# Optimization experiments

Hardware: AMD Instinct MI355X
Metric: run time of the kernel (lower is better)

Reference implementation:

```python
import jax, jax.numpy as jnp
import numpy as np

NEG = -1e6  # mask fill value used by d2l.sequence_mask


def setup_inputs() -> dict:
    key = jax.random.key(0)
    k1, k2, k3, k4, k5, k6, k7 = jax.random.split(key, 7)
    B, Q, K, DQ, DK, H, DV = 8, 256, 1024, 256, 256, 128, 128
    queries = jax.random.normal(k1, (B, Q, DQ), dtype=jnp.float32)
    keys = jax.random.normal(k2, (B, K, DK), dtype=jnp.float32)
    values = jax.random.normal(k3, (B, K, DV), dtype=jnp.float32)
    valid_lens = jax.random.randint(k4, (B,), 1, K + 1, dtype=jnp.int32)
    # learned params (nn.Linear stores weight as [out, in]; apply as x @ W.T)
    W_q = jax.random.normal(k5, (H, DQ), dtype=jnp.float32) / np.sqrt(DQ)
    W_k = jax.random.normal(k6, (H, DK), dtype=jnp.float32) / np.sqrt(DK)
    w_v = jax.random.normal(k7, (H,), dtype=jnp.float32) / np.sqrt(H)
    return {"queries": queries, "keys": keys, "values": values,
            "valid_lens": valid_lens, "W_q": W_q, "W_k": W_k, "w_v": w_v}


def reference(queries, keys, values, valid_lens, W_q, W_k, w_v):
    # projections
    q = jnp.einsum('bqd,hd->bqh', queries, W_q)   # [B,Q,H]
    k = jnp.einsum('bkd,hd->bkh', keys, W_k)      # [B,K,H]
    # broadcast add + tanh -> [B,Q,K,H] (the fusion-headroom intermediate)
    features = jnp.tanh(q[:, :, None, :] + k[:, None, :, :])
    scores = jnp.einsum('bqkh,h->bqk', features, w_v)  # [B,Q,K]
    # masked softmax: valid_lens is per-batch (dim==1 path)
    klen = scores.shape[-1]
    mask = jnp.arange(klen)[None, None, :] < valid_lens[:, None, None]
    scores = jnp.where(mask, scores, NEG)
    weights = jax.nn.softmax(scores, axis=-1)
    # dropout is identity in eval mode
    return jnp.einsum('bqk,bkv->bqv', weights, values)
```

## Files before the change

### kernel.cpp

```cpp
#include <hip/hip_runtime.h>


#define Bb 8
#define Qn 256
#define Kk 1024
#define Dd 256
#define Hh 128
#define DVv 128

__device__ __forceinline__ float fexp2(float x) { return __builtin_amdgcn_exp2f(x); }
__device__ __forceinline__ float frcp(float x)  { return __builtin_amdgcn_rcpf(x); }

__global__ __launch_bounds__(256)
void repack_w(const float* __restrict__ Wq, const float* __restrict__ Wk,
              float4* __restrict__ Wq4T, float4* __restrict__ Wk4T)
{
    const int blk = blockIdx.x;
    const float* src = (blk < 32) ? Wq : Wk;
    float4*      dst = (blk < 32) ? Wq4T : Wk4T;
    const int idx = (blk & 31) * 256 + threadIdx.x;
    const int g = idx >> 7;
    const int h = idx & 127;
    dst[idx] = *(const float4*)(src + (size_t)h * Dd + g * 4);
}

__global__ __launch_bounds__(512)
void proj_exp_kernel(const float* __restrict__ queries,
                     const float* __restrict__ keys,
                     const float4* __restrict__ Wq4T,
                     const float4* __restrict__ Wk4T,
                     float* __restrict__ EqT,
                     float* __restrict__ EkT)
{
    __shared__ __align__(16) float Xs[16 * 256];
    const int blk = blockIdx.x;
    const float* X; const float4* W4; float* outT; int RB; int i0;
    if (blk < 128) { X = queries; W4 = Wq4T; outT = EqT; RB = Qn; i0 = blk * 16; }
    else           { X = keys;    W4 = Wk4T; outT = EkT; RB = Kk; i0 = (blk - 128) * 16; }
    const int tid = threadIdx.x;
    const int h   = tid & 127;
    const int r4  = __builtin_amdgcn_readfirstlane(tid >> 7);

    {
        const float4* xsrc = (const float4*)(X + (size_t)i0 * Dd);
#pragma unroll
        for (int s = 0; s < 2; ++s) {
            const int idx = tid + 512 * s;
            *(float4*)(Xs + idx * 4) = xsrc[idx];
        }
    }
    __syncthreads();

    float acc[4] = {0.f, 0.f, 0.f, 0.f};
    const float4* wp = W4 + h;
    const float*  xr = Xs + (r4 * 4) * 256;
#pragma unroll 8
    for (int g = 0; g < 64; ++g) {
        const float4 w = wp[(size_t)g * 128];
#pragma unroll
        for (int i = 0; i < 4; ++i) {
            const float4 x = *(const float4*)(xr + i * 256 + g * 4);
            acc[i] = fmaf(x.x, w.x, acc[i]);
            acc[i] = fmaf(x.y, w.y, acc[i]);
            acc[i] = fmaf(x.z, w.z, acc[i]);
            acc[i] = fmaf(x.w, w.w, acc[i]);
        }
    }
    const int b    = i0 / RB;
    const int rloc = (i0 % RB) + r4 * 4;
    float4 o;
    o.x = fexp2(acc[0] * 2.885390082f);
    o.y = fexp2(acc[1] * 2.885390082f);
    o.z = fexp2(acc[2] * 2.885390082f);
    o.w = fexp2(acc[3] * 2.885390082f);
    *(float4*)(outT + (size_t)b * Hh * RB + (size_t)h * RB + rloc) = o;
}

__global__ __launch_bounds__(512, 8)
void score_softmax_pv_kernel(const float* __restrict__ EqT,
                             const float* __restrict__ EkT,
                             const float* __restrict__ wv,
                             const int* __restrict__ valid_lens,
                             const float* __restrict__ values,
                             float* __restrict__ out)
{
    __shared__ __align__(16) float  s_sc[4][Kk];
    __shared__ __align__(16) float  eqsT[4][Hh];
    __shared__ __align__(16) float  w2s[Hh];
    __shared__ __align__(16) float4 s_part[7][4][32];
    __shared__ float s_qmax[4][2];
    __shared__ float s_qsum[4][2];

    const int blk  = blockIdx.x;
    const int b    = blk & 7;
    const int qt   = blk >> 3;
    const int q0   = qt * 4;
    const int len  = valid_lens[b];
    const int tid  = threadIdx.x;
    const int lane = tid & 63;
    const int wave = __builtin_amdgcn_readfirstlane(tid >> 6);

    if (tid < 128) {
        const float4 v = *(const float4*)(EqT + (size_t)b * Hh * Qn + (size_t)tid * Qn + q0);
        eqsT[0][tid] = v.x; eqsT[1][tid] = v.y; eqsT[2][tid] = v.z; eqsT[3][tid] = v.w;
    } else if (tid < 256) {
        w2s[tid - 128] = -2.0f * wv[tid - 128];
    }
    __syncthreads();

    const int kspan = (tid >> 6) << 7;
    if (kspan < len) {
        const float2* ek2 = (const float2*)(EkT + (size_t)b * Hh * Kk) + tid;
        float acc[4][2] = {};
#pragma unroll 2
        for (int hg = 0; hg < 32; ++hg) {
            const int h = hg << 2;
            const float2 e0 = ek2[(size_t)(h + 0) * (Kk / 2)];
            const float2 e1 = ek2[(size_t)(h + 1) * (Kk / 2)];
            const float2 e2 = ek2[(size_t)(h + 2) * (Kk / 2)];
            const float2 e3 = ek2[(size_t)(h + 3) * (Kk / 2)];
            const float4 w4 = *(const float4*)(w2s + h);
#pragma unroll
            for (int q = 0; q < 4; ++q) {
                const float4 q4 = *(const float4*)(&eqsT[q][h]);
                {
                    const float A = fmaf(q4.x, e0.x, 1.f), B = fmaf(q4.y, e1.x, 1.f);
                    const float C = fmaf(q4.z, e2.x, 1.f), E = fmaf(q4.w, e3.x, 1.f);
                    const float AB = A * B, CE = C * E;
                    const float N = fmaf(fmaf(w4.x, B, w4.y * A), CE,
                                         fmaf(w4.z, E, w4.w * C) * AB);
                    acc[q][0] = fmaf(N, frcp(AB * CE), acc[q][0]);
                }
                {
                    const float A = fmaf(q4.x, e0.y, 1.f), B = fmaf(q4.y, e1.y, 1.f);
                    const float C = fmaf(q4.z, e2.y, 1.f), E = fmaf(q4.w, e3.y, 1.f);
                    const float AB = A * B, CE = C * E;
                    const float N = fmaf(fmaf(w4.x, B, w4.y * A), CE,
                                         fmaf(w4.z, E, w4.w * C) * AB);
                    acc[q][1] = fmaf(N, frcp(AB * CE), acc[q][1]);
                }
            }
        }
#pragma unroll
        for (int q = 0; q < 4; ++q)
            *(float2*)(&s_sc[q][tid << 1]) = make_float2(acc[q][0], acc[q][1]);
    }
    __syncthreads();

    {
        const int q    = wave & 3;
        const int half = wave >> 2;
        const int base = half * 512;
        const int hi   = (base + 512 < len) ? base + 512 : len;
        float m = -3.0e38f;
        for (int i = base + lane; i < hi; i += 64) m = fmaxf(m, s_sc[q][i]);
#pragma unroll
        for (int off = 32; off > 0; off >>= 1) m = fmaxf(m, __shfl_xor(m, off));
        if (lane == 0) s_qmax[q][half] = m;
        __syncthreads();
        const float gm = fmaxf(s_qmax[q][0], s_qmax[q][1]);
        float sum = 0.f;
        for (int i = base + lane; i < hi; i += 64) {
            const float p = fexp2((s_sc[q][i] - gm) * 1.44269504f);
            s_sc[q][i] = p;
            sum += p;
        }
#pragma unroll
        for (int off = 32; off > 0; off >>= 1) sum += __shfl_xor(sum, off);
        if (lane == 0) s_qsum[q][half] = sum;
    }
    __syncthreads();

    {
        const int slice = tid >> 5;
        const int l32   = tid & 31;
        const int v4    = l32 << 2;
        const float* vp = values + (size_t)b * Kk * DVv + v4;
        float a[4][4];
#pragma unroll
        for (int q = 0; q < 4; ++q) { a[q][0]=0.f; a[q][1]=0.f; a[q][2]=0.f; a[q][3]=0.f; }
        for (int k = slice; k < len; k += 16) {
            const float4 val = *(const float4*)(vp + (size_t)k * DVv);
            const float w0 = s_sc[0][k], w1 = s_sc[1][k], w2 = s_sc[2][k], w3 = s_sc[3][k];
            a[0][0] = fmaf(w0, val.x, a[0][0]);
            a[0][1] = fmaf(w0, val.y, a[0][1]);
            a[0][2] = fmaf(w0, val.z, a[0][2]);
            a[0][3] = fmaf(w0, val.w, a[0][3]);
            a[1][0] = fmaf(w1, val.x, a[1][0]);
            a[1][1] = fmaf(w1, val.y, a[1][1]);
            a[1][2] = fmaf(w1, val.z, a[1][2]);
            a[1][3] = fmaf(w1, val.w, a[1][3]);
            a[2][0] = fmaf(w2, val.x, a[2][0]);
            a[2][1] = fmaf(w2, val.y, a[2][1]);
            a[2][2] = fmaf(w2, val.z, a[2][2]);
            a[2][3] = fmaf(w2, val.w, a[2][3]);
            a[3][0] = fmaf(w3, val.x, a[3][0]);
            a[3][1] = fmaf(w3, val.y, a[3][1]);
            a[3][2] = fmaf(w3, val.z, a[3][2]);
            a[3][3] = fmaf(w3, val.w, a[3][3]);
        }
#pragma unroll
        for (int q = 0; q < 4; ++q)
#pragma unroll
            for (int x = 0; x < 4; ++x) a[q][x] += __shfl_xor(a[q][x], 32);
        if (wave > 0 && lane < 32) {
#pragma unroll
            for (int q = 0; q < 4; ++q)
                s_part[wave - 1][q][l32] = make_float4(a[q][0], a[q][1], a[q][2], a[q][3]);
        }
        __syncthreads();
        if (wave == 0 && lane < 32) {
#pragma unroll
            for (int q = 0; q < 4; ++q) {
                float r0 = a[q][0], r1 = a[q][1], r2 = a[q][2], r3 = a[q][3];
#pragma unroll
                for (int w = 0; w < 7; ++w) {
                    const float4 p = s_part[w][q][l32];
                    r0 += p.x; r1 += p.y; r2 += p.z; r3 += p.w;
                }
                const float inv = frcp(s_qsum[q][0] + s_qsum[q][1]);
                *(float4*)(out + (size_t)(b * Qn + q0 + q) * DVv + v4) =
                    make_float4(r0 * inv, r1 * inv, r2 * inv, r3 * inv);
            }
        }
    }
}

extern "C" void kernel_launch(void* const* d_in, const int* in_sizes, int n_in,
                              void* d_out, int out_size, void* d_ws, size_t ws_size,
                              hipStream_t stream) {
    (void)in_sizes; (void)n_in; (void)out_size; (void)ws_size;
    const float* queries    = (const float*)d_in[0];
    const float* keys       = (const float*)d_in[1];
    const float* values     = (const float*)d_in[2];
    const int*   valid_lens = (const int*)  d_in[3];
    const float* Wq         = (const float*)d_in[4];
    const float* Wk         = (const float*)d_in[5];
    const float* wvv        = (const float*)d_in[6];
    float* out = (float*)d_out;

    float* Wq4T = (float*)d_ws;
    float* Wk4T = Wq4T + (size_t)Dd * Hh;
    float* EqT  = Wk4T + (size_t)Dd * Hh;
    float* EkT  = EqT + (size_t)Bb * Hh * Qn;

    repack_w       <<<  64, 256, 0, stream>>>(Wq, Wk, (float4*)Wq4T, (float4*)Wk4T);
    proj_exp_kernel<<< 640, 512, 0, stream>>>(queries, keys, (const float4*)Wq4T,
                                              (const float4*)Wk4T, EqT, EkT);
    score_softmax_pv_kernel<<<512, 512, 0, stream>>>(EqT, EkT, wvv, valid_lens,
                                                     values, out);
}
```

Before: 134.4 us.

## Stage key projections through double-buffered LDS chunks in score kernel

The score phase now streams the transposed key projections through a double-buffered shared-memory tile of 16 h-rows by 256 keys, prefetching the next chunk into registers while computing the current one. The thread mapping changes from each thread computing 2 keys for 4 queries to each thread computing 1 key for 2 queries, and the partial-reduction buffer is aliased onto the new tile. The aim is to overlap global loads with the tanh-product math and cut per-thread register pressure. In exchange it adds a block-wide barrier per chunk, larger LDS use, and a lower occupancy hint.

```diff
diff --git a/kernel.cpp b/kernel.cpp
--- a/kernel.cpp
+++ b/kernel.cpp
@@ -76,7 +76,7 @@
     *(float4*)(outT + (size_t)b * Hh * RB + (size_t)h * RB + rloc) = o;
 }
 
-__global__ __launch_bounds__(512, 8)
+__global__ __launch_bounds__(512, 6)
 void score_softmax_pv_kernel(const float* __restrict__ EqT,
                              const float* __restrict__ EkT,
                              const float* __restrict__ wv,
@@ -84,12 +84,13 @@
                              const float* __restrict__ values,
                              float* __restrict__ out)
 {
-    __shared__ __align__(16) float  s_sc[4][Kk];
-    __shared__ __align__(16) float  eqsT[4][Hh];
-    __shared__ __align__(16) float  w2s[Hh];
-    __shared__ __align__(16) float4 s_part[7][4][32];
+    __shared__ __align__(16) float s_sc[4][Kk];
+    __shared__ __align__(16) float eks[2][16][256];
+    __shared__ __align__(16) float eqsT[4][Hh];
+    __shared__ __align__(16) float w2s[Hh];
     __shared__ float s_qmax[4][2];
     __shared__ float s_qsum[4][2];
+    float4 (*s_part)[4][32] = (float4 (*)[4][32])(&eks[0][0][0]);
 
     const int blk  = blockIdx.x;
     const int b    = blk & 7;
@@ -106,46 +107,78 @@
     } else if (tid < 256) {
         w2s[tid - 128] = -2.0f * wv[tid - 128];
     }
+
+    const int nch  = ((len + 255) >> 8) << 3;
+    const int kloc = tid & 255;
+    const int qh2  = (tid >> 8) << 1;
+    const float* ekg = EkT + (size_t)b * Hh * Kk;
+
+    {
+#pragma unroll
+        for (int j = 0; j < 2; ++j) {
+            const int s = tid + (j << 9);
+            const int row = s >> 6, col = (s & 63) << 2;
+            *(float4*)(&eks[0][row][col]) = *(const float4*)(ekg + (size_t)row * Kk + col + s * 0);
+        }
+    }
     __syncthreads();
 
-    const int kspan = (tid >> 6) << 7;
-    if (kspan < len) {
-        const float2* ek2 = (const float2*)(EkT + (size_t)b * Hh * Kk) + tid;
-        float acc[4][2] = {};
-#pragma unroll 2
-        for (int hg = 0; hg < 32; ++hg) {
-            const int h = hg << 2;
-            const float2 e0 = ek2[(size_t)(h + 0) * (Kk / 2)];
-            const float2 e1 = ek2[(size_t)(h + 1) * (Kk / 2)];
-            const float2 e2 = ek2[(size_t)(h + 2) * (Kk / 2)];
-            const float2 e3 = ek2[(size_t)(h + 3) * (Kk / 2)];
-            const float4 w4 = *(const float4*)(w2s + h);
-#pragma unroll
-            for (int q = 0; q < 4; ++q) {
-                const float4 q4 = *(const float4*)(&eqsT[q][h]);
+    float acc0 = 0.f, acc1 = 0.f;
+    for (int c = 0; c < nch; ++c) {
+        float4 st0, st1;
+        const bool more = (c + 1 < nch);
+        if (more) {
+            const int kb2 = ((c + 1) >> 3) << 8;
+            const int h02 = ((c + 1) & 7) << 4;
+            const int s0 = tid, s1 = tid + 512;
+            st0 = *(const float4*)(ekg + (size_t)(h02 + (s0 >> 6)) * Kk + kb2 + ((s0 & 63) << 2));
+            st1 = *(const float4*)(ekg + (size_t)(h02 + (s1 >> 6)) * Kk + kb2 + ((s1 & 63) << 2));
+        }
+        {
+            const int h0 = (c & 7) << 4;
+            const float* ek = &eks[c & 1][0][kloc];
+#pragma unroll
+            for (int hg = 0; hg < 4; ++hg) {
+                const int hl = hg << 2;
+                const float e0 = ek[(hl + 0) << 8];
+                const float e1 = ek[(hl + 1) << 8];
+                const float e2 = ek[(hl + 2) << 8];
+                const float e3 = ek[(hl + 3) << 8];
+                const int h = h0 + hl;
+                const float4 w4 = *(const float4*)(w2s + h);
                 {
-                    const float A = fmaf(q4.x, e0.x, 1.f), B = fmaf(q4.y, e1.x, 1.f);
-                    const float C = fmaf(q4.z, e2.x, 1.f), E = fmaf(q4.w, e3.x, 1.f);
+                    const float4 q4 = *(const float4*)(&eqsT[qh2][h]);
+                    const float A = fmaf(q4.x, e0, 1.f), B = fmaf(q4.y, e1, 1.f);
+                    const float C = fmaf(q4.z, e2, 1.f), E = fmaf(q4.w, e3, 1.f);
                     const float AB = A * B, CE = C * E;
                     const float N = fmaf(fmaf(w4.x, B, w4.y * A), CE,
                                          fmaf(w4.z, E, w4.w * C) * AB);
-                    acc[q][0] = fmaf(N, frcp(AB * CE), acc[q][0]);
+                    acc0 = fmaf(N, frcp(AB * CE), acc0);
                 }
                 {
-                    const float A = fmaf(q4.x, e0.y, 1.f), B = fmaf(q4.y, e1.y, 1.f);
-                    const float C = fmaf(q4.z, e2.y, 1.f), E = fmaf(q4.w, e3.y, 1.f);
+                    const float4 q4 = *(const float4*)(&eqsT[qh2 + 1][h]);
+                    const float A = fmaf(q4.x, e0, 1.f), B = fmaf(q4.y, e1, 1.f);
+                    const float C = fmaf(q4.z, e2, 1.f), E = fmaf(q4.w, e3, 1.f);
                     const float AB = A * B, CE = C * E;
                     const float N = fmaf(fmaf(w4.x, B, w4.y * A), CE,
                                          fmaf(w4.z, E, w4.w * C) * AB);
-                    acc[q][1] = fmaf(N, frcp(AB * CE), acc[q][1]);
+                    acc1 = fmaf(N, frcp(AB * CE), acc1);
                 }
             }
-        }
-#pragma unroll
-        for (int q = 0; q < 4; ++q)
-            *(float2*)(&s_sc[q][tid << 1]) = make_float2(acc[q][0], acc[q][1]);
-    }
-    __syncthreads();
+            if ((c & 7) == 7) {
+                const int k = ((c >> 3) << 8) + kloc;
+                s_sc[qh2][k]     = acc0;
+                s_sc[qh2 + 1][k] = acc1;
+                acc0 = 0.f; acc1 = 0.f;
+            }
+        }
+        if (more) {
+            float* dst = &eks[(c + 1) & 1][0][0];
+            *(float4*)(dst + ((tid >> 6) << 8) + ((tid & 63) << 2)) = st0;
+            *(float4*)(dst + (((tid + 512) >> 6) << 8) + ((tid & 63) << 2)) = st1;
+        }
+        __syncthreads();
+    }
 
     {
         const int q    = wave & 3;
```

Result: slower. 162.3 us (+20.8%).
